# Optimization experiments

Hardware: AMD Instinct MI355X
Metric: run time of the kernel (lower is better)

## Reference

```python
import jax, jax.numpy as jnp
import numpy as np

NUM_HEADS = 32
NUM_KV_HEADS = 8
HEAD_DIM = 128
HIDDEN = 4096
ROPE_THETA = 10000.0
SLIDING_WINDOW = 1024
NEG_INF = -1e9


def _make_sliding_window_mask(q_len, kv_len, window):
    # additive mask: 0 where attendable (causal AND within window), -inf otherwise
    i = jnp.arange(q_len)[:, None]
    j = jnp.arange(kv_len)[None, :]
    allowed = (j <= i) & (j > i - window)
    return jnp.where(allowed, 0.0, NEG_INF).astype(jnp.float32)[None, None]  # [1,1,q,kv]


def _rope_tables(seq_len, head_dim, theta):
    inv_freq = 1.0 / (theta ** (jnp.arange(0, head_dim, 2, dtype=jnp.float32) / head_dim))
    t = jnp.arange(seq_len, dtype=jnp.float32)
    freqs = jnp.einsum('i,j->ij', t, inv_freq)        # [S, D/2]
    emb = jnp.concatenate([freqs, freqs], axis=-1)     # [S, D]
    return jnp.cos(emb), jnp.sin(emb)


def _rotate_half(x):
    d = x.shape[-1] // 2
    return jnp.concatenate([-x[..., d:], x[..., :d]], axis=-1)


def setup_inputs() -> dict:
    key = jax.random.key(0)
    ks = jax.random.split(key, 5)
    B, S = 1, 2048
    sc = 0.02
    hidden_states = jax.random.normal(ks[0], (B, S, HIDDEN), dtype=jnp.float32)
    Wq = jax.random.normal(ks[1], (HIDDEN, NUM_HEADS * HEAD_DIM), dtype=jnp.float32) * sc
    Wk = jax.random.normal(ks[2], (HIDDEN, NUM_KV_HEADS * HEAD_DIM), dtype=jnp.float32) * sc
    Wv = jax.random.normal(ks[3], (HIDDEN, NUM_KV_HEADS * HEAD_DIM), dtype=jnp.float32) * sc
    Wo = jax.random.normal(ks[4], (NUM_HEADS * HEAD_DIM, HIDDEN), dtype=jnp.float32) * sc
    attention_mask = _make_sliding_window_mask(S, S, SLIDING_WINDOW)
    position_ids = jnp.arange(S, dtype=jnp.int64)[None, :]
    return {"hidden_states": hidden_states, "attention_mask": attention_mask,
            "position_ids": position_ids, "Wq": Wq, "Wk": Wk, "Wv": Wv, "Wo": Wo}


def reference(hidden_states, attention_mask, position_ids, Wq, Wk, Wv, Wo):
    B, S, _ = hidden_states.shape
    # projections
    q = (hidden_states @ Wq).reshape(B, S, NUM_HEADS, HEAD_DIM).transpose(0, 2, 1, 3)      # [B,H,S,D]
    k = (hidden_states @ Wk).reshape(B, S, NUM_KV_HEADS, HEAD_DIM).transpose(0, 2, 1, 3)   # [B,Hk,S,D]
    v = (hidden_states @ Wv).reshape(B, S, NUM_KV_HEADS, HEAD_DIM).transpose(0, 2, 1, 3)
    # RoPE
    cos_t, sin_t = _rope_tables(S, HEAD_DIM, ROPE_THETA)
    cos = cos_t[position_ids][:, None]  # [B,1,S,D]
    sin = sin_t[position_ids][:, None]
    q = q * cos + _rotate_half(q) * sin
    k = k * cos + _rotate_half(k) * sin
    # repeat_kv (GQA): [B,Hk,S,D] -> [B,H,S,D]
    n_rep = NUM_HEADS // NUM_KV_HEADS
    k = jnp.repeat(k, n_rep, axis=1)
    v = jnp.repeat(v, n_rep, axis=1)
    # attention
    scores = jnp.einsum('bhqd,bhkd->bhqk', q, k) / np.sqrt(HEAD_DIM)
    scores = scores + attention_mask
    probs = jax.nn.softmax(scores, axis=-1)
    out = jnp.einsum('bhqk,bhkd->bhqd', probs, v)
    out = out.transpose(0, 2, 1, 3).reshape(B, S, HIDDEN)
    return out @ Wo
```

## Files before the change

kernel.cpp:

```cpp
#include <hip/hip_runtime.h>

typedef __attribute__((ext_vector_type(8))) short short8;
typedef __attribute__((ext_vector_type(4))) short s16x4;
typedef __attribute__((ext_vector_type(4))) float f32x4;
typedef unsigned short u16;
typedef unsigned int u32;

__device__ __forceinline__ u16 f2bf(float f) {
  union { float f; unsigned int u; } v; v.f = f;
  unsigned int r = (v.u + 0x7FFFu + ((v.u >> 16) & 1u)) >> 16;
  return (u16)r;
}
__device__ __forceinline__ float bf2f(u16 b) {
  union { unsigned int u; float f; } v; v.u = ((unsigned int)b) << 16;
  return v.f;
}
__device__ __forceinline__ void load_lds16(const void* g, void* l) {
  __builtin_amdgcn_global_load_lds((const __attribute__((address_space(1))) void*)g,
                                   (__attribute__((address_space(3))) void*)l, 16, 0, 0);
}

__device__ __forceinline__ void tconv64_tile(const float* __restrict__ W, u16* __restrict__ Wt,
                                             int K, int N, int nb, int kb, int tid) {
  __shared__ float tile[64][65];
  int tx = tid & 15, ty = tid >> 4;
  const float* src = W + (size_t)(kb + ty) * N + nb + tx * 4;
#pragma unroll
  for (int i = 0; i < 4; ++i) {
    float4 v = *(const float4*)(src + (size_t)i * 16 * N);
    tile[ty + i * 16][tx * 4 + 0] = v.x;
    tile[ty + i * 16][tx * 4 + 1] = v.y;
    tile[ty + i * 16][tx * 4 + 2] = v.z;
    tile[ty + i * 16][tx * 4 + 3] = v.w;
  }
  __syncthreads();
  u16* dst = Wt + (size_t)(nb + ty) * K + kb + tx * 4;
#pragma unroll
  for (int i = 0; i < 4; ++i) {
    s16x4 o;
#pragma unroll
    for (int j = 0; j < 4; ++j) o[j] = (short)f2bf(tile[tx * 4 + j][ty + i * 16]);
    *(s16x4*)(dst + (size_t)i * 16 * K) = o;
  }
}

__global__ void prep_kernel(const float* __restrict__ Wq, const float* __restrict__ Wk,
                            const float* __restrict__ Wv, u16* __restrict__ WqT,
                            u16* __restrict__ WkvT, const float* __restrict__ X,
                            u16* __restrict__ Xb, float* __restrict__ Tab) {
  int id = blockIdx.x;
  int tid = threadIdx.x;
  if (id < 4096) { tconv64_tile(Wq, WqT, 4096, 4096, (id & 63) * 64, (id >> 6) * 64, tid); return; }
  if (id < 5120) { int t = id - 4096; tconv64_tile(Wk, WkvT, 4096, 1024, (t & 15) * 64, (t >> 4) * 64, tid); return; }
  if (id < 6144) { int t = id - 5120; tconv64_tile(Wv, WkvT + (size_t)1024 * 4096, 4096, 1024, (t & 15) * 64, (t >> 4) * 64, tid); return; }
  if (id < 14336) {
    int i = (id - 6144) * 256 + tid;
    float4 v = ((const float4*)X)[i];
    ushort4 o;
    o.x = f2bf(v.x); o.y = f2bf(v.y); o.z = f2bf(v.z); o.w = f2bf(v.w);
    ((ushort4*)Xb)[i] = o;
    return;
  }
  {
    int i = (id - 14336) * 256 + tid;
    int s = i >> 6, j = i & 63;
    float invf = exp2f(-(float)j * (13.287712379549449f / 64.0f));
    float sn, cs;
    sincosf((float)s * invf, &sn, &cs);
    Tab[(size_t)s * 128 + j * 2]     = cs;
    Tab[(size_t)s * 128 + j * 2 + 1] = sn;
  }
}

__global__ void tconv1_kernel(const float* __restrict__ W, u16* __restrict__ Wt) {
  int id = blockIdx.x;
  tconv64_tile(W, Wt, 4096, 4096, (id & 63) * 64, (id >> 6) * 64, threadIdx.x);
}

__global__ void combine2_f32_kernel(float* __restrict__ out, const u16* __restrict__ p0,
                                    const u16* __restrict__ p1, int n8) {
  int i = blockIdx.x * blockDim.x + threadIdx.x;
  if (i >= n8) return;
  short8 a = ((const short8*)p0)[i];
  short8 b = ((const short8*)p1)[i];
  float4 o0, o1;
  o0.x = bf2f((u16)a[0]) + bf2f((u16)b[0]);
  o0.y = bf2f((u16)a[1]) + bf2f((u16)b[1]);
  o0.z = bf2f((u16)a[2]) + bf2f((u16)b[2]);
  o0.w = bf2f((u16)a[3]) + bf2f((u16)b[3]);
  o1.x = bf2f((u16)a[4]) + bf2f((u16)b[4]);
  o1.y = bf2f((u16)a[5]) + bf2f((u16)b[5]);
  o1.z = bf2f((u16)a[6]) + bf2f((u16)b[6]);
  o1.w = bf2f((u16)a[7]) + bf2f((u16)b[7]);
  ((float4*)out)[i * 2]     = o0;
  ((float4*)out)[i * 2 + 1] = o1;
}

__global__ void combine_kv_rope_kernel(const u16* __restrict__ PKV, u16* __restrict__ Kb,
                                       u16* __restrict__ Vt, const float* __restrict__ Tab) {
  int i = blockIdx.x * blockDim.x + threadIdx.x;
  if (i < 131072) {
    int s = i >> 6, r = i & 63, hh = r >> 3, c = r & 7;
    size_t lo8 = (size_t)s * 128 + hh * 16 + c;
    size_t hi8 = lo8 + 8;
    float lo[8] = {0,0,0,0,0,0,0,0}, hi[8] = {0,0,0,0,0,0,0,0};
#pragma unroll
    for (int z = 0; z < 4; ++z) {
      short8 a = *(const short8*)(PKV + (size_t)z * 4194304 + lo8 * 8);
      short8 b = *(const short8*)(PKV + (size_t)z * 4194304 + hi8 * 8);
#pragma unroll
      for (int j = 0; j < 8; ++j) { lo[j] += bf2f((u16)a[j]); hi[j] += bf2f((u16)b[j]); }
    }
    const float* tr = Tab + (size_t)s * 128 + c * 16;
    short8 olo, ohi;
#pragma unroll
    for (int ii = 0; ii < 8; ++ii) {
      float cs = tr[ii * 2], sn = tr[ii * 2 + 1];
      olo[ii] = (short)f2bf(lo[ii] * cs - hi[ii] * sn);
      ohi[ii] = (short)f2bf(hi[ii] * cs + lo[ii] * sn);
    }
    *(short8*)(Kb + lo8 * 8) = olo;
    *(short8*)(Kb + hi8 * 8) = ohi;
  } else {
    int v = i - 131072;
    const u16* src = PKV + 2097152;
    float sm[8] = {0,0,0,0,0,0,0,0};
#pragma unroll
    for (int z = 0; z < 4; ++z) {
      short8 a = *(const short8*)(src + (size_t)z * 4194304 + (size_t)v * 8);
#pragma unroll
      for (int j = 0; j < 8; ++j) sm[j] += bf2f((u16)a[j]);
    }
    short8 o;
#pragma unroll
    for (int j = 0; j < 8; ++j) o[j] = (short)f2bf(sm[j]);
    ((short8*)Vt)[v] = o;
  }
}

__global__ __launch_bounds__(512, 1) void gemm256_kernel(
    const u16* __restrict__ A, const u16* __restrict__ B,
    u16* __restrict__ C0, u16* __restrict__ C1, int N, int K, int KH) {
  __shared__ u16 As[2][256 * 64];
  __shared__ u16 Bs[2][256 * 64];
  int tid = threadIdx.x, lane = tid & 63, wid = tid >> 6;
  int wr = wid >> 2, wc = wid & 3;
  int g = lane >> 4, q = lane & 15;
  int id = blockIdx.z * gridDim.x * gridDim.y + blockIdx.y * gridDim.x + blockIdx.x;
  int tot = gridDim.x * gridDim.y * gridDim.z;
  int swz = (id & 7) * (tot >> 3) + (id >> 3);
  int perh = gridDim.x * gridDim.y;
  int z = swz / perh, rem = swz % perh;
  int m0 = (rem / gridDim.x) * 256, n0 = (rem % gridDim.x) * 256;
  int k0 = z * KH;
  f32x4 acc[8][4];
#pragma unroll
  for (int i = 0; i < 8; ++i)
#pragma unroll
    for (int j = 0; j < 4; ++j) acc[i][j] = (f32x4){0.f, 0.f, 0.f, 0.f};
  int srow = tid >> 3;
  int scol = ((tid & 7) ^ (srow & 7)) << 3;
  const u16* ga = A + (size_t)(m0 + srow) * K + k0 + scol;
  const u16* gb = B + (size_t)(n0 + srow) * K + k0 + scol;
  int xorm = (q & 7) << 3;
  int arow = wr * 128 + q;
  int brow = wc * 64 + q;
  int nt = KH >> 6;

  auto stage = [&](int buf, int t) {
    const u16* pa = ga + t * 64;
    const u16* pb = gb + t * 64;
#pragma unroll
    for (int it = 0; it < 4; ++it) {
      load_lds16(pa + (size_t)it * 64 * K, (char*)(&As[buf][0]) + it * 8192 + tid * 16);
      load_lds16(pb + (size_t)it * 64 * K, (char*)(&Bs[buf][0]) + it * 8192 + tid * 16);
    }
  };

  stage(0, 0);
  stage(1, 1);
  asm volatile("s_waitcnt vmcnt(8)" ::: "memory");
  __builtin_amdgcn_s_barrier();
  for (int t = 0; t < nt; ++t) {
    int cur = t & 1;
    int col0 = (g * 8) ^ xorm;
    short8 a0[8], b0[4];
#pragma unroll
    for (int m = 0; m < 8; ++m) a0[m] = *(const short8*)&As[cur][(arow + m * 16) * 64 + col0];
#pragma unroll
    for (int n = 0; n < 4; ++n) b0[n] = *(const short8*)&Bs[cur][(brow + n * 16) * 64 + col0];
    __builtin_amdgcn_s_setprio(1);
#pragma unroll
    for (int m = 0; m < 8; ++m)
#pragma unroll
      for (int n = 0; n < 4; ++n)
        acc[m][n] = __builtin_amdgcn_mfma_f32_16x16x32_bf16(a0[m], b0[n], acc[m][n], 0, 0, 0);
    __builtin_amdgcn_s_setprio(0);
    int col1 = (32 + g * 8) ^ xorm;
    short8 a1[8], b1[4];
#pragma unroll
    for (int m = 0; m < 8; ++m) a1[m] = *(const short8*)&As[cur][(arow + m * 16) * 64 + col1];
#pragma unroll
    for (int n = 0; n < 4; ++n) b1[n] = *(const short8*)&Bs[cur][(brow + n * 16) * 64 + col1];
    asm volatile("s_waitcnt lgkmcnt(0)" ::: "memory");
    __builtin_amdgcn_s_barrier();
    if (t + 2 < nt) stage(cur, t + 2);
    __builtin_amdgcn_sched_barrier(0);
    __builtin_amdgcn_s_setprio(1);
#pragma unroll
    for (int m = 0; m < 8; ++m)
#pragma unroll
      for (int n = 0; n < 4; ++n)
        acc[m][n] = __builtin_amdgcn_mfma_f32_16x16x32_bf16(a1[m], b1[n], acc[m][n], 0, 0, 0);
    __builtin_amdgcn_s_setprio(0);
    if (t + 2 < nt)      { asm volatile("s_waitcnt vmcnt(8)" ::: "memory"); }
    else if (t + 1 < nt) { asm volatile("s_waitcnt vmcnt(0)" ::: "memory"); }
    __builtin_amdgcn_s_barrier();
  }
  int crow = m0 + wr * 128 + g * 4;
  int ccol = n0 + wc * 64 + q;
  u16* dst = z ? C1 : C0;
#pragma unroll
  for (int fm = 0; fm < 8; ++fm)
#pragma unroll
    for (int fn = 0; fn < 4; ++fn)
#pragma unroll
      for (int r = 0; r < 4; ++r)
        dst[(size_t)(crow + fm * 16 + r) * N + ccol + fn * 16] = f2bf(acc[fm][fn][r]);
}

__global__ __launch_bounds__(512, 1) void gemm_kv256_kernel(
    const u16* __restrict__ A, const u16* __restrict__ B,
    u16* __restrict__ PKV, int K, int KH) {
  __shared__ u16 As[2][256 * 64];
  __shared__ u16 Bs[2][256 * 64];
  int tid = threadIdx.x, lane = tid & 63, wid = tid >> 6;
  int wr = wid >> 2, wc = wid & 3;
  int g = lane >> 4, q = lane & 15;
  int id = blockIdx.z * 64 + blockIdx.y * 8 + blockIdx.x;
  int swz = (id & 7) * 32 + (id >> 3);
  int z = swz >> 6, rem = swz & 63;
  int m0 = (rem >> 3) * 256, n0 = (rem & 7) * 256;
  int k0 = z * KH;
  f32x4 acc[8][4];
#pragma unroll
  for (int i = 0; i < 8; ++i)
#pragma unroll
    for (int j = 0; j < 4; ++j) acc[i][j] = (f32x4){0.f, 0.f, 0.f, 0.f};
  int srow = tid >> 3;
  int scol = ((tid & 7) ^ (srow & 7)) << 3;
  const u16* ga = A + (size_t)(m0 + srow) * K + k0 + scol;
  const u16* gb = B + (size_t)(n0 + srow) * K + k0 + scol;
  int xorm = (q & 7) << 3;
  int arow = wr * 128 + q;
  int brow = wc * 64 + q;
  int nt = KH >> 6;

  auto stage = [&](int buf, int t) {
    const u16* pa = ga + t * 64;
    const u16* pb = gb + t * 64;
#pragma unroll
    for (int it = 0; it < 4; ++it) {
      load_lds16(pa + (size_t)it * 64 * K, (char*)(&As[buf][0]) + it * 8192 + tid * 16);
      load_lds16(pb + (size_t)it * 64 * K, (char*)(&Bs[buf][0]) + it * 8192 + tid * 16);
    }
  };

  stage(0, 0);
  stage(1, 1);
  asm volatile("s_waitcnt vmcnt(8)" ::: "memory");
  __builtin_amdgcn_s_barrier();
  for (int t = 0; t < nt; ++t) {
    int cur = t & 1;
    int col0 = (g * 8) ^ xorm;
    short8 a0[8], b0[4];
#pragma unroll
    for (int m = 0; m < 8; ++m) a0[m] = *(const short8*)&As[cur][(arow + m * 16) * 64 + col0];
#pragma unroll
    for (int n = 0; n < 4; ++n) b0[n] = *(const short8*)&Bs[cur][(brow + n * 16) * 64 + col0];
    __builtin_amdgcn_s_setprio(1);
#pragma unroll
    for (int m = 0; m < 8; ++m)
#pragma unroll
      for (int n = 0; n < 4; ++n)
        acc[m][n] = __builtin_amdgcn_mfma_f32_16x16x32_bf16(a0[m], b0[n], acc[m][n], 0, 0, 0);
    __builtin_amdgcn_s_setprio(0);
    int col1 = (32 + g * 8) ^ xorm;
    short8 a1[8], b1[4];
#pragma unroll
    for (int m = 0; m < 8; ++m) a1[m] = *(const short8*)&As[cur][(arow + m * 16) * 64 + col1];
#pragma unroll
    for (int n = 0; n < 4; ++n) b1[n] = *(const short8*)&Bs[cur][(brow + n * 16) * 64 + col1];
    asm volatile("s_waitcnt lgkmcnt(0)" ::: "memory");
    __builtin_amdgcn_s_barrier();
    if (t + 2 < nt) stage(cur, t + 2);
    __builtin_amdgcn_sched_barrier(0);
    __builtin_amdgcn_s_setprio(1);
#pragma unroll
    for (int m = 0; m < 8; ++m)
#pragma unroll
      for (int n = 0; n < 4; ++n)
        acc[m][n] = __builtin_amdgcn_mfma_f32_16x16x32_bf16(a1[m], b1[n], acc[m][n], 0, 0, 0);
    __builtin_amdgcn_s_setprio(0);
    if (t + 2 < nt)      { asm volatile("s_waitcnt vmcnt(8)" ::: "memory"); }
    else if (t + 1 < nt) { asm volatile("s_waitcnt vmcnt(0)" ::: "memory"); }
    __builtin_amdgcn_s_barrier();
  }
  int crow = m0 + wr * 128 + g * 4;
  int ccol = n0 + wc * 64 + q;
  u16* Kpart = PKV + (size_t)z * 4194304;
  u16* Vpart = Kpart + 2097152;
  if (n0 < 1024) {
#pragma unroll
    for (int fm = 0; fm < 8; ++fm)
#pragma unroll
      for (int fn = 0; fn < 4; ++fn)
#pragma unroll
        for (int r = 0; r < 4; ++r)
          Kpart[(size_t)(crow + fm * 16 + r) * 1024 + ccol + fn * 16] = f2bf(acc[fm][fn][r]);
  } else {
#pragma unroll
    for (int fn = 0; fn < 4; ++fn) {
      int vcol = ccol + fn * 16 - 1024;
#pragma unroll
      for (int fm = 0; fm < 8; ++fm) {
        s16x4 o;
#pragma unroll
        for (int r = 0; r < 4; ++r) o[r] = (short)f2bf(acc[fm][fn][r]);
        *(s16x4*)(Vpart + (size_t)vcol * 2048 + crow + fm * 16) = o;
      }
    }
  }
}

__global__ __launch_bounds__(512, 4) void attn_kernel(
    const u16* __restrict__ Q0, const u16* __restrict__ Q1,
    const u16* __restrict__ Kg, const u16* __restrict__ Vt,
    const float* __restrict__ Tab, u16* __restrict__ O) {
  __shared__ u16 Ks[2][64 * 128];
  __shared__ u16 Vs[2][128 * 64];
  __shared__ u16 Ps[8][16 * 64];
  int tid = threadIdx.x, lane = tid & 63, w = tid >> 6;
  int wg = w >> 2;
  int g = lane >> 4, q = lane & 15;
  int q0 = blockIdx.x * 128;
  int h = blockIdx.y, hk = h >> 2;
  int qbase = q0 + wg * 64;
  int qrow = qbase + (w & 3) * 16;
  int xorm = (lane & 7) << 3;
  int bjt_lo = (q0 >= 1024) ? ((q0 - 1023) >> 6) : 0;
  int bjt_hi = (q0 + 64) >> 6;
  int wjt_lo = (qbase >= 1024) ? ((qbase - 1023) >> 6) : 0;
  int wjt_hi = qbase >> 6;
  int krow = tid >> 4;
  int kchunk = (tid & 15) ^ (krow & 7);
  const u16* kbase = Kg + (size_t)krow * 1024 + hk * 128 + (kchunk << 3);
  int vrow = tid >> 3;
  int vchunk = (tid & 7) ^ (vrow & 7);
  const u16* vbase = Vt + (size_t)(hk * 128 + vrow) * 2048 + (vchunk << 3);

  auto stageK = [&](int buf, int j0) {
    const u16* gp = kbase + (size_t)j0 * 1024;
#pragma unroll
    for (int it = 0; it < 2; ++it)
      load_lds16(gp + (size_t)it * 32 * 1024, (char*)(&Ks[buf][0]) + it * 8192 + tid * 16);
  };
  auto stageV = [&](int buf, int j0) {
    const u16* gp = vbase + j0;
#pragma unroll
    for (int it = 0; it < 2; ++it)
      load_lds16(gp + (size_t)it * 64 * 2048, (char*)(&Vs[buf][0]) + it * 8192 + tid * 16);
  };

  stageK(0, bjt_lo << 6);
  stageV(0, bjt_lo << 6);
  short8 qf[4];
  {
    size_t qoff = (size_t)(qrow + q) * 4096 + h * 128 + g * 8;
    float sum[4][8];
#pragma unroll
    for (int kk = 0; kk < 4; ++kk) {
      short8 a = *(const short8*)(Q0 + qoff + kk * 32);
      short8 b = *(const short8*)(Q1 + qoff + kk * 32);
#pragma unroll
      for (int i = 0; i < 8; ++i) sum[kk][i] = bf2f((u16)a[i]) + bf2f((u16)b[i]);
    }
    const float scale = 0.12751781828987514f;
    const float* tr = Tab + (size_t)(qrow + q) * 128;
#pragma unroll
    for (int kk = 0; kk < 2; ++kk)
#pragma unroll
      for (int i = 0; i < 8; ++i) {
        int j = kk * 32 + g * 8 + i;
        float cs = tr[j * 2], sn = tr[j * 2 + 1];
        float lo = sum[kk][i], hi = sum[kk + 2][i];
        qf[kk][i]     = (short)f2bf((lo * cs - hi * sn) * scale);
        qf[kk + 2][i] = (short)f2bf((hi * cs + lo * sn) * scale);
      }
  }
  float mrow = -1e30f, lsum = 0.f;
  f32x4 of[8];
#pragma unroll
  for (int d = 0; d < 8; ++d) of[d] = (f32x4){0.f, 0.f, 0.f, 0.f};

  u16* pl = &Ps[w][(size_t)q * 64];

  int cur = 0;
  asm volatile("s_waitcnt vmcnt(0)" ::: "memory");
  __syncthreads();
  for (int jt = bjt_lo; jt <= bjt_hi; ++jt) {
    int j0 = jt << 6;
    if (jt < bjt_hi) { stageK(cur ^ 1, j0 + 64); stageV(cur ^ 1, j0 + 64); }
    if (jt >= wjt_lo && jt <= wjt_hi) {
      f32x4 sf[4];
#pragma unroll
      for (int nt = 0; nt < 4; ++nt) sf[nt] = (f32x4){0.f, 0.f, 0.f, 0.f};
      const u16* ks = &Ks[cur][0];
      __builtin_amdgcn_s_setprio(1);
#pragma unroll
      for (int kk = 0; kk < 4; ++kk) {
        short8 qv = qf[kk];
        int col = (kk * 32 + g * 8) ^ xorm;
#pragma unroll
        for (int nt = 0; nt < 4; ++nt) {
          short8 kf = *(const short8*)&ks[(nt * 16 + q) * 128 + col];
          sf[nt] = __builtin_amdgcn_mfma_f32_16x16x32_bf16(kf, qv, sf[nt], 0, 0, 0);
        }
      }
      __builtin_amdgcn_s_setprio(0);
      float p[4][4];
#pragma unroll
      for (int nt = 0; nt < 4; ++nt)
#pragma unroll
        for (int r = 0; r < 4; ++r) p[nt][r] = sf[nt][r];
      if (j0 + 63 > qrow || j0 + 1009 <= qrow) {
        int qq = qrow + q;
        int kb = j0 + g * 4;
#pragma unroll
        for (int nt = 0; nt < 4; ++nt)
#pragma unroll
          for (int r = 0; r < 4; ++r) {
            int key = kb + nt * 16 + r;
            if (key > qq || key + 1024 <= qq) p[nt][r] = -1e9f;
          }
      }
      float tm = p[0][0];
#pragma unroll
      for (int nt = 0; nt < 4; ++nt)
#pragma unroll
        for (int r = 0; r < 4; ++r) tm = fmaxf(tm, p[nt][r]);
      tm = fmaxf(tm, __shfl_xor(tm, 16));
      tm = fmaxf(tm, __shfl_xor(tm, 32));
      if (__any(tm > mrow + 8.f)) {
        float nm = fmaxf(mrow, tm);
        float sc = __builtin_amdgcn_exp2f(mrow - nm);
        mrow = nm;
        lsum *= sc;
#pragma unroll
        for (int d = 0; d < 8; ++d) of[d] *= sc;
      }
      float ps = 0.f;
#pragma unroll
      for (int nt = 0; nt < 4; ++nt)
#pragma unroll
        for (int r = 0; r < 4; ++r) {
          float e = __builtin_amdgcn_exp2f(p[nt][r] - mrow);
          p[nt][r] = e;
          ps += e;
        }
      ps += __shfl_xor(ps, 16);
      ps += __shfl_xor(ps, 32);
      lsum += ps;
#pragma unroll
      for (int nt = 0; nt < 4; ++nt) {
        u32 u0 = __builtin_amdgcn_perm(__float_as_uint(p[nt][1]), __float_as_uint(p[nt][0]), 0x07060302u);
        u32 u1 = __builtin_amdgcn_perm(__float_as_uint(p[nt][3]), __float_as_uint(p[nt][2]), 0x07060302u);
        int col = (nt * 16 + g * 4) ^ xorm;
        union { u32 u[2]; double d; } wv;
        wv.u[0] = u0; wv.u[1] = u1;
        *(double*)&pl[col] = wv.d;
      }
      asm volatile("s_waitcnt lgkmcnt(0)" ::: "memory");
      const u16* vs = &Vs[cur][0];
      __builtin_amdgcn_s_setprio(1);
#pragma unroll
      for (int kh = 0; kh < 2; ++kh) {
        short8 pb = *(const short8*)&pl[(kh * 32 + g * 8) ^ xorm];
        int col = (kh * 32 + g * 8) ^ xorm;
#pragma unroll
        for (int dt = 0; dt < 8; ++dt) {
          short8 vv = *(const short8*)&vs[(dt * 16 + q) * 64 + col];
          of[dt] = __builtin_amdgcn_mfma_f32_16x16x32_bf16(vv, pb, of[dt], 0, 0, 0);
        }
      }
      __builtin_amdgcn_s_setprio(0);
    }
    asm volatile("s_waitcnt vmcnt(0)" ::: "memory");
    __builtin_amdgcn_s_barrier();
    cur ^= 1;
  }
  float inv = 1.f / lsum;
  u16* op = O + (size_t)(qrow + q) * 4096 + h * 128 + g * 4;
#pragma unroll
  for (int dt = 0; dt < 8; ++dt) {
    s16x4 o4;
#pragma unroll
    for (int r = 0; r < 4; ++r) o4[r] = (short)f2bf(of[dt][r] * inv);
    *(s16x4*)(op + dt * 16) = o4;
  }
}

extern "C" void kernel_launch(void* const* d_in, const int* in_sizes, int n_in,
                              void* d_out, int out_size, void* d_ws, size_t ws_size,
                              hipStream_t stream) {
  (void)in_sizes; (void)n_in; (void)out_size;
  const float* hs = (const float*)d_in[0];
  const float* Wq = (const float*)d_in[3];
  const float* Wk = (const float*)d_in[4];
  const float* Wv = (const float*)d_in[5];
  const float* Wo = (const float*)d_in[6];
  float* out = (float*)d_out;
  char* ws = (char*)d_ws;

  u16* Xb   = (u16*)(ws + 0);
  u16* Wt   = (u16*)(ws + 16777216);
  u16* WkvT = (u16*)(ws + 50331648);
  u16* Qb   = (u16*)(ws + 67108864);
  u16* Kb   = (u16*)(ws + 83886080);
  u16* Vtb  = (u16*)(ws + 88080384);
  float* Tab = (float*)(ws + 92274688);
  u16* P1q  = (u16*)(ws + 96468992);
  u16* PKV  = Wt;
  u16* P0o  = WkvT;
  u16* P1o  = Qb;
  u16* Ao   = Xb;
  if (ws_size < 113246208u) return;

  prep_kernel<<<dim3(14848), 256, 0, stream>>>(Wq, Wk, Wv, Wt, WkvT, hs, Xb, Tab);

  gemm256_kernel<<<dim3(16, 8, 2), 512, 0, stream>>>(Xb, Wt, Qb, P1q, 4096, 4096, 2048);

  gemm_kv256_kernel<<<dim3(8, 8, 4), 512, 0, stream>>>(Xb, WkvT, PKV, 4096, 1024);
  combine_kv_rope_kernel<<<dim3(1536), 256, 0, stream>>>(PKV, Kb, Vtb, Tab);

  attn_kernel<<<dim3(16, 32), 512, 0, stream>>>(Qb, P1q, Kb, Vtb, Tab, Ao);

  tconv1_kernel<<<dim3(4096), 256, 0, stream>>>(Wo, Wt);
  gemm256_kernel<<<dim3(16, 8, 2), 512, 0, stream>>>(Ao, Wt, P0o, P1o, 4096, 4096, 2048);
  combine2_f32_kernel<<<dim3(4096), 256, 0, stream>>>(out, P0o, P1o, 1048576);
}
```

Before: 294.3 us.

## Fuse Wo transpose-convert into attention launch to overlap with attention

Merges the separate Wo transpose/bf16-convert kernel into the attention kernel launch. The first 512 blocks run attention and the extra 2048 blocks each convert two 64x64 tiles of Wo, so this memory-bound conversion can fill idle CUs alongside attention and one launch is removed. The cost is a shared-memory union buffer and a flattened 1D grid. Those extra blocks also compete with attention blocks for CU resources.

```diff
diff --git a/kernel.cpp b/kernel.cpp
--- a/kernel.cpp
+++ b/kernel.cpp
@@ -40,6 +40,30 @@
     s16x4 o;
 #pragma unroll
     for (int j = 0; j < 4; ++j) o[j] = (short)f2bf(tile[tx * 4 + j][ty + i * 16]);
+    *(s16x4*)(dst + (size_t)i * 16 * K) = o;
+  }
+}
+
+__device__ __forceinline__ void tconv64_tile_p(const float* __restrict__ W, u16* __restrict__ Wt,
+                                               int K, int N, int nb, int kb, int tid,
+                                               float* __restrict__ tile) {
+  int tx = tid & 15, ty = tid >> 4;
+  const float* src = W + (size_t)(kb + ty) * N + nb + tx * 4;
+#pragma unroll
+  for (int i = 0; i < 4; ++i) {
+    float4 v = *(const float4*)(src + (size_t)i * 16 * N);
+    tile[(ty + i * 16) * 65 + tx * 4 + 0] = v.x;
+    tile[(ty + i * 16) * 65 + tx * 4 + 1] = v.y;
+    tile[(ty + i * 16) * 65 + tx * 4 + 2] = v.z;
+    tile[(ty + i * 16) * 65 + tx * 4 + 3] = v.w;
+  }
+  __syncthreads();
+  u16* dst = Wt + (size_t)(nb + ty) * K + kb + tx * 4;
+#pragma unroll
+  for (int i = 0; i < 4; ++i) {
+    s16x4 o;
+#pragma unroll
+    for (int j = 0; j < 4; ++j) o[j] = (short)f2bf(tile[(tx * 4 + j) * 65 + ty + i * 16]);
     *(s16x4*)(dst + (size_t)i * 16 * K) = o;
   }
 }
@@ -70,11 +94,6 @@
     Tab[(size_t)s * 128 + j * 2]     = cs;
     Tab[(size_t)s * 128 + j * 2 + 1] = sn;
   }
-}
-
-__global__ void tconv1_kernel(const float* __restrict__ W, u16* __restrict__ Wt) {
-  int id = blockIdx.x;
-  tconv64_tile(W, Wt, 4096, 4096, (id & 63) * 64, (id >> 6) * 64, threadIdx.x);
 }
 
 __global__ void combine2_f32_kernel(float* __restrict__ out, const u16* __restrict__ p0,
@@ -333,18 +352,27 @@
   }
 }
 
-__global__ __launch_bounds__(512, 4) void attn_kernel(
+__global__ __launch_bounds__(512, 4) void attn_tconv_kernel(
     const u16* __restrict__ Q0, const u16* __restrict__ Q1,
     const u16* __restrict__ Kg, const u16* __restrict__ Vt,
-    const float* __restrict__ Tab, u16* __restrict__ O) {
-  __shared__ u16 Ks[2][64 * 128];
-  __shared__ u16 Vs[2][128 * 64];
-  __shared__ u16 Ps[8][16 * 64];
-  int tid = threadIdx.x, lane = tid & 63, w = tid >> 6;
+    const float* __restrict__ Tab, u16* __restrict__ O,
+    const float* __restrict__ Wo, u16* __restrict__ WoT) {
+  __shared__ char sbuf[81920];
+  int tid = threadIdx.x;
+  if (blockIdx.x >= 512) {
+    int t2 = (blockIdx.x - 512) * 2 + (tid >> 8);
+    float* tile = (float*)(sbuf + (tid >> 8) * 16640);
+    tconv64_tile_p(Wo, WoT, 4096, 4096, (t2 & 63) * 64, (t2 >> 6) * 64, tid & 255, tile);
+    return;
+  }
+  u16 (*Ks)[8192] = (u16(*)[8192])sbuf;
+  u16 (*Vs)[8192] = (u16(*)[8192])(sbuf + 32768);
+  u16 (*Ps)[1024] = (u16(*)[1024])(sbuf + 65536);
+  int lane = tid & 63, w = tid >> 6;
   int wg = w >> 2;
   int g = lane >> 4, q = lane & 15;
-  int q0 = blockIdx.x * 128;
-  int h = blockIdx.y, hk = h >> 2;
+  int q0 = (blockIdx.x & 15) * 128;
+  int h = blockIdx.x >> 4, hk = h >> 2;
   int qbase = q0 + wg * 64;
   int qrow = qbase + (w & 3) * 16;
   int xorm = (lane & 7) << 3;
@@ -543,9 +571,8 @@
   gemm_kv256_kernel<<<dim3(8, 8, 4), 512, 0, stream>>>(Xb, WkvT, PKV, 4096, 1024);
   combine_kv_rope_kernel<<<dim3(1536), 256, 0, stream>>>(PKV, Kb, Vtb, Tab);
 
-  attn_kernel<<<dim3(16, 32), 512, 0, stream>>>(Qb, P1q, Kb, Vtb, Tab, Ao);
-
-  tconv1_kernel<<<dim3(4096), 256, 0, stream>>>(Wo, Wt);
+  attn_tconv_kernel<<<dim3(2560), 512, 0, stream>>>(Qb, P1q, Kb, Vtb, Tab, Ao, Wo, Wt);
+
   gemm256_kernel<<<dim3(16, 8, 2), 512, 0, stream>>>(Ao, Wt, P0o, P1o, 4096, 4096, 2048);
   combine2_f32_kernel<<<dim3(4096), 256, 0, stream>>>(out, P0o, P1o, 1048576);
 }
```

Result: faster. 285.1 us (-3.1%).
